# Kernel tuning notes

Hardware: AMD Instinct MI355X
Metric: run time of the kernel (lower is better)

## Reference

```python
import jax, jax.numpy as jnp
import numpy as np

B, S, D, NQ, NC, MC, K = 64, 200, 128, 50000, 1000, 4, 10
N = NQ + NC  # total graph nodes (concepts first, then questions, matching torch concat order)


def setup_inputs() -> dict:
    key = jax.random.key(0)
    ks = jax.random.split(key, 32)
    f = lambda i, shape: jax.random.normal(ks[i], shape, dtype=jnp.float32) * 0.02
    return {
        "emb_q": f(0, (NQ, D)), "emb_c": f(1, (NC, D)), "emb_r": f(2, (2, D)),
        "Wih1": f(3, (3 * D, 2 * D)), "Whh1": f(4, (3 * D, D)), "bih1": f(5, (3 * D,)), "bhh1": f(6, (3 * D,)),
        "Wih2": f(7, (3 * D, D)), "Whh2": f(8, (3 * D, D)), "bih2": f(9, (3 * D,)), "bhh2": f(10, (3 * D,)),
        "Wg1": f(11, (D, D)), "Wg2": f(12, (D, D)), "Wg3": f(13, (D, D)),
        "Wagg": f(14, (D, D)), "bagg": f(15, (D,)),
        "Wq": f(16, (D, D)), "bq": f(17, (D,)),
        "Wk": f(18, (D, D)), "bk": f(19, (D,)),
        "Ww": f(20, (1, 2 * D)), "bw": f(21, (1,)),
        "question_seq": jax.random.randint(ks[22], (B, S), 0, NQ),
        "correct_seq": jax.random.randint(ks[23], (B, S), 0, 2),
        "mask_seq": jnp.ones((B, S), dtype=jnp.int32),
        "q_table": jax.random.randint(ks[24], (NQ, MC), 0, NC),
    }


def _gru(x, h, Wih, Whh, bih, bhh):
    gi = x @ Wih.T + bih
    gh = h @ Whh.T + bhh
    i_r, i_z, i_n = jnp.split(gi, 3, axis=-1)
    h_r, h_z, h_n = jnp.split(gh, 3, axis=-1)
    r = jax.nn.sigmoid(i_r + h_r)
    z = jax.nn.sigmoid(i_z + h_z)
    n = jnp.tanh(i_n + r * h_n)
    return (1.0 - z) * n + z * h


def _sage_mean(x, src, dst, W):
    # SAGEConv4GIKT (eval): out = lin_r(mean_agg_over_neighbors + x), lin_r has no bias.
    agg = jax.ops.segment_sum(x[dst], src, num_segments=N)
    cnt = jax.ops.segment_sum(jnp.ones((src.shape[0], 1), x.dtype), src, num_segments=N)
    agg = agg / jnp.maximum(cnt, 1.0)
    return (agg + x) @ W.T


def reference(emb_q, emb_c, emb_r, Wih1, Whh1, bih1, bhh1, Wih2, Whh2, bih2, bhh2,
              Wg1, Wg2, Wg3, Wagg, bagg, Wq, bq, Wk, bk, Ww, bw,
              question_seq, correct_seq, mask_seq, q_table):
    # ---- GNN propagation over the full question-concept bipartite graph ----
    x = jnp.concatenate([emb_c, emb_q], axis=0)  # [N, D], concepts first
    q_glob = jnp.repeat(jnp.arange(NQ, dtype=q_table.dtype) + NC, MC)  # question global ids
    c_glob = q_table.reshape(-1)                                       # concept global ids
    x = _sage_mean(x, q_glob, c_glob, Wg1)  # q2c: aggregate at questions from concepts
    x = _sage_mean(x, c_glob, q_glob, Wg2)  # c2q: aggregate at concepts from questions
    x = _sage_mean(x, q_glob, c_glob, Wg3)  # q2c again
    x = jnp.tanh(x @ Wagg.T + bagg)

    tgrid = jnp.arange(S)

    def step(carry, inp):
        h1, h2, keyhist, statehist = carry
        t, q_t, r_t, m_t, q_next = inp
        m = (m_t != 0)[:, None]
        e_q = jnp.where(m, x[q_t + NC], emb_q[q_t])  # GNN emb where masked-in, raw emb otherwise
        e_r = emb_r[r_t]
        h1 = _gru(jnp.concatenate([e_q, e_r], axis=1), h1, Wih1, Whh1, bih1, bhh1)
        h2 = _gru(h1, h2, Wih2, Whh2, bih2, bhh2)
        statehist = statehist.at[:, t].set(h2)
        keyhist = keyhist.at[:, t].set(h2 @ Wk.T + bk)
        # queries: next question emb + its concept embs -> [B, MC+1, D]
        qc = jnp.concatenate([emb_q[q_next][:, None, :], emb_c[q_table[q_next]]], axis=1)
        aq = qc @ Wq.T + bq
        scores = jnp.einsum('bid,bjd->bij', aq, keyhist)  # [B, MC+1, S]
        scores = jnp.where((tgrid <= t)[None, None, :], scores, -1e9)
        flat = scores.reshape(B, -1)
        vals, idx = jax.lax.top_k(flat, K)  # top-k (query, state) pairs
        alpha = jax.nn.softmax(vals, axis=-1)
        i_idx = idx // S
        j_idx = idx % S
        q_sel = jnp.take_along_axis(qc, i_idx[:, :, None], axis=1)        # [B, K, D]
        s_sel = jnp.take_along_axis(statehist, j_idx[:, :, None], axis=1)  # [B, K, D]
        f = jax.nn.sigmoid(jnp.concatenate([q_sel, s_sel], axis=-1) @ Ww.T + bw)[..., 0]
        y = jnp.sum(alpha * f, axis=-1)  # [B]
        return (h1, h2, keyhist, statehist), y

    h0 = jnp.zeros((B, D), jnp.float32)
    carry = (h0, h0, jnp.zeros((B, S, D), jnp.float32), jnp.zeros((B, S, D), jnp.float32))
    xs = (jnp.arange(S - 1), question_seq[:, :-1].T, correct_seq[:, :-1].T,
          mask_seq[:, :-1].T, question_seq[:, 1:].T)
    _, ys = jax.lax.scan(step, carry, xs)
    y_hat = jnp.concatenate([jnp.zeros((B, 1), jnp.float32), ys.T], axis=1)  # predictions for t=1..S-1
    return y_hat
```

## Files before the change

### kernel.cpp

```cpp
#include <hip/hip_runtime.h>
#include <math.h>

#define Bz 64
#define Sz 200
#define Dz 128
#define NQz 50000
#define NCz 1000
#define MCz 4
#define Kz 10
#define Tz 199
#define NSz (Bz*Tz)
#define NEz (NQz*MCz)

__global__ void k_count(const int* __restrict__ qt, int* __restrict__ cnt) {
    int e = blockIdx.x*256 + threadIdx.x;
    if (e < NEz) atomicAdd(&cnt[qt[e]], 1);
}

__global__ void k_offs(const int* __restrict__ cnt, int* __restrict__ offs) {
    __shared__ int s[1024];
    int tid = threadIdx.x;
    s[tid] = (tid < NCz) ? cnt[tid] : 0;
    __syncthreads();
    for (int off = 1; off < 1024; off <<= 1) {
        int add = (tid >= off) ? s[tid - off] : 0;
        __syncthreads();
        s[tid] += add;
        __syncthreads();
    }
    if (tid < NCz) offs[tid + 1] = s[tid];
    if (tid == 0) offs[0] = 0;
}

__global__ void k_fill(const int* __restrict__ qt, const int* __restrict__ offs,
                       int* __restrict__ fill, int* __restrict__ edge_q) {
    int e = blockIdx.x*256 + threadIdx.x;
    if (e < NEz) {
        int c = qt[e];
        int pos = atomicAdd(&fill[c], 1);
        edge_q[offs[c] + pos] = e >> 2;
    }
}

__global__ void k_m2(const int* __restrict__ qt, const int* __restrict__ offs,
                     const int* __restrict__ edge_q,
                     const float* __restrict__ emb_q, const float* __restrict__ emb_c,
                     float* __restrict__ m2) {
    int c = blockIdx.x;
    int g = threadIdx.x >> 7;
    int d = threadIdx.x & 127;
    int e0 = offs[c], e1 = offs[c+1];
    float acc = 0.f;
    for (int e = e0 + g; e < e1; e += 4) {
        int q = edge_q[e];
        const int* t4 = qt + q*4;
        int c0 = t4[0], c1 = t4[1], c2 = t4[2], c3 = t4[3];
        acc += emb_q[q*128 + d]
             + 0.25f*(emb_c[c0*128+d] + emb_c[c1*128+d] + emb_c[c2*128+d] + emb_c[c3*128+d]);
    }
    __shared__ float ps[4][128];
    ps[g][d] = acc;
    __syncthreads();
    if (g == 0) {
        float tot = ps[0][d] + ps[1][d] + ps[2][d] + ps[3][d];
        float cn = (float)(e1 - e0);
        m2[c*128 + d] = tot / fmaxf(cn, 1.0f);
    }
}

template<bool TR>
__global__ void k_mm128(const float* __restrict__ X, const float* __restrict__ Y,
                        float* __restrict__ out) {
    int r = blockIdx.x, c = threadIdx.x;
    float acc = 0.f;
    for (int e = 0; e < 128; ++e) acc += X[r*128 + e] * Y[e*128 + c];
    if (TR) out[c*128 + r] = acc;
    else    out[r*128 + c] = acc;
}

__global__ void k_gr(const float* __restrict__ emb_r, const float* __restrict__ Wih1,
                     const float* __restrict__ bih1, float* __restrict__ gr) {
    int rt = threadIdx.x / 384, r = threadIdx.x % 384;
    float acc = bih1[r];
    for (int e = 0; e < 128; ++e) acc += emb_r[rt*128 + e] * Wih1[r*256 + 128 + e];
    gr[rt*384 + r] = acc;
}

__global__ void k_bkq(const float* __restrict__ Wq, const float* __restrict__ Wk,
                      const float* __restrict__ bq, const float* __restrict__ bk,
                      const float* __restrict__ Ww, const float* __restrict__ bw,
                      float* __restrict__ Bkq, float* __restrict__ biaskq) {
    int r = blockIdx.x, d = threadIdx.x;
    if (r < 128) {
        float acc = 0.f;
        for (int n = 0; n < 128; ++n) acc += Wq[n*128 + r] * Wk[n*128 + d];
        Bkq[r*128 + d] = acc;
        if (d == 0) {
            float b0 = 0.f;
            for (int n = 0; n < 128; ++n) b0 += Wq[n*128 + r] * bk[n];
            biaskq[r] = b0;
        }
    } else if (r == 128) {
        float acc = 0.f;
        for (int n = 0; n < 128; ++n) acc += bq[n] * Wk[n*128 + d];
        Bkq[128*128 + d] = acc;
        if (d == 0) {
            float c0 = 0.f;
            for (int n = 0; n < 128; ++n) c0 += bq[n] * bk[n];
            biaskq[128] = c0;
        }
    } else {
        Bkq[129*128 + d] = Ww[128 + d];
        if (d == 0) biaskq[129] = bw[0];
    }
}

__global__ void k_eq(const float* __restrict__ Mt_g, const float* __restrict__ bagg,
                     const float* __restrict__ emb_q, const float* __restrict__ emb_c,
                     const float* __restrict__ m2, const int* __restrict__ qseq,
                     const int* __restrict__ mseq, const int* __restrict__ qt,
                     float* __restrict__ eq) {
    __shared__ float Mt[128*128];
    __shared__ float ub[2][128];
    int tid = threadIdx.x;
    for (int i = tid; i < 128*128/4; i += 256)
        ((float4*)Mt)[i] = ((const float4*)Mt_g)[i];
    __syncthreads();
    int g = tid >> 7, d = tid & 127;
    for (int it = 0; it < 8; ++it) {
        int slot = blockIdx.x*16 + it*2 + g;
        int b = slot / Tz, t = slot % Tz;
        int q = qseq[b*Sz + t];
        int msk = mseq[b*Sz + t];
        if (msk) {
            const int* t4 = qt + q*4;
            int c0 = t4[0], c1 = t4[1], c2 = t4[2], c3 = t4[3];
            ub[g][d] = emb_q[q*128 + d]
                     + 0.5f *(emb_c[c0*128+d] + emb_c[c1*128+d] + emb_c[c2*128+d] + emb_c[c3*128+d])
                     + 0.25f*(m2[c0*128+d]  + m2[c1*128+d]  + m2[c2*128+d]  + m2[c3*128+d]);
        }
        __syncthreads();
        if (msk) {
            float acc = bagg[d];
            const float* urow = ub[g];
            for (int e = 0; e < 128; ++e) acc += Mt[e*128 + d] * urow[e];
            eq[slot*128 + d] = tanhf(acc);
        } else {
            eq[slot*128 + d] = emb_q[q*128 + d];
        }
        __syncthreads();
    }
}

__device__ __forceinline__ float bf_lo(unsigned u){ return __uint_as_float(u << 16); }
__device__ __forceinline__ float bf_hi(unsigned u){ return __uint_as_float(u & 0xffff0000u); }
__device__ __forceinline__ unsigned f2bf(float x){
    unsigned u = __float_as_uint(x);
    return (u + 0x7fffu + ((u >> 16) & 1u)) >> 16;
}
__device__ __forceinline__ unsigned pk2(float a, float b){
    return f2bf(a) | (f2bf(b) << 16);
}
__device__ __forceinline__ float rcpf(float x){ return __builtin_amdgcn_rcpf(x); }
__device__ __forceinline__ float sigm(float x){ return rcpf(1.f + __expf(-x)); }
__device__ __forceinline__ float tanh_fast(float x){
    float e = __expf(2.f*x);
    return 1.f - 2.f*rcpf(e + 1.f);
}

#if __has_builtin(__builtin_amdgcn_fdot2_f32_bf16)
typedef __attribute__((ext_vector_type(2))) short short2v;
__device__ __forceinline__ float bdot2(unsigned w, unsigned h, float acc) {
    return __builtin_amdgcn_fdot2_f32_bf16(__builtin_bit_cast(short2v, w),
                                           __builtin_bit_cast(short2v, h), acc, false);
}
#else
__device__ __forceinline__ float bdot2(unsigned w, unsigned h, float acc) {
    return acc + bf_lo(w)*bf_lo(h) + bf_hi(w)*bf_hi(h);
}
#endif

template<int MODE, int DOT2>
__global__ void k_gemm(const float* __restrict__ A, const float* __restrict__ Bm,
                       int ldb, int nB, float* __restrict__ C, int ldc,
                       const float* __restrict__ bias, const float* __restrict__ gr,
                       const int* __restrict__ cseq) {
    __shared__ int rtb[64];
    int tx = threadIdx.x, ty = threadIdx.y;
    int tid = ty*16 + tx;
    int m0 = blockIdx.x * 64;
    int n0 = blockIdx.y * 64;
    if (MODE == 1 && tid < 64) {
        int s = m0 + tid;
        int b = s / Tz, t = s % Tz;
        rtb[tid] = cseq[b*Sz + t];
    }
    float acc[4][4];
    #pragma unroll
    for (int i = 0; i < 4; ++i)
        #pragma unroll
        for (int j = 0; j < 4; ++j) acc[i][j] = 0.f;

    if (DOT2) {
        __shared__ unsigned As[64][17];
        __shared__ unsigned Bs[64][17];
        for (int kc = 0; kc < 128; kc += 32) {
            #pragma unroll
            for (int l = 0; l < 2; ++l) {
                int v = tid*2 + l;
                int row = v >> 3, c4 = (v & 7) << 2;
                int p0 = (kc + c4) >> 1 & 15;
                float4 av = *(const float4*)(A + (size_t)(m0+row)*128 + kc + c4);
                As[row][p0]   = pk2(av.x, av.y);
                As[row][p0+1] = pk2(av.z, av.w);
                int nrow = n0 + row;
                float4 bv = make_float4(0.f, 0.f, 0.f, 0.f);
                if (nrow < nB) bv = *(const float4*)(Bm + (size_t)nrow*ldb + kc + c4);
                Bs[row][p0]   = pk2(bv.x, bv.y);
                Bs[row][p0+1] = pk2(bv.z, bv.w);
            }
            __syncthreads();
            #pragma unroll 4
            for (int kp = 0; kp < 16; ++kp) {
                unsigned av[4], bv[4];
                #pragma unroll
                for (int i = 0; i < 4; ++i) av[i] = As[ty*4+i][kp];
                #pragma unroll
                for (int j = 0; j < 4; ++j) bv[j] = Bs[tx*4+j][kp];
                #pragma unroll
                for (int i = 0; i < 4; ++i)
                    #pragma unroll
                    for (int j = 0; j < 4; ++j) acc[i][j] = bdot2(av[i], bv[j], acc[i][j]);
            }
            __syncthreads();
        }
    } else {
        __shared__ float Asf[64][33];
        __shared__ float Bsf[64][33];
        for (int kc = 0; kc < 128; kc += 32) {
            #pragma unroll
            for (int l = 0; l < 2; ++l) {
                int v = tid*2 + l;
                int row = v >> 3, c4 = (v & 7) << 2;
                float4 av = *(const float4*)(A + (size_t)(m0+row)*128 + kc + c4);
                Asf[row][c4+0] = av.x; Asf[row][c4+1] = av.y; Asf[row][c4+2] = av.z; Asf[row][c4+3] = av.w;
                int nrow = n0 + row;
                float4 bv = make_float4(0.f, 0.f, 0.f, 0.f);
                if (nrow < nB) bv = *(const float4*)(Bm + (size_t)nrow*ldb + kc + c4);
                Bsf[row][c4+0] = bv.x; Bsf[row][c4+1] = bv.y; Bsf[row][c4+2] = bv.z; Bsf[row][c4+3] = bv.w;
            }
            __syncthreads();
            #pragma unroll 8
            for (int k = 0; k < 32; ++k) {
                float av[4], bv[4];
                #pragma unroll
                for (int i = 0; i < 4; ++i) av[i] = Asf[ty*4+i][k];
                #pragma unroll
                for (int j = 0; j < 4; ++j) bv[j] = Bsf[tx*4+j][k];
                #pragma unroll
                for (int i = 0; i < 4; ++i)
                    #pragma unroll
                    for (int j = 0; j < 4; ++j) acc[i][j] += av[i]*bv[j];
            }
            __syncthreads();
        }
    }
    #pragma unroll
    for (int i = 0; i < 4; ++i) {
        int s = m0 + ty*4 + i;
        #pragma unroll
        for (int j = 0; j < 4; ++j) {
            int col = n0 + tx*4 + j;
            if (col < nB) {
                float v = acc[i][j];
                if (MODE == 0) v += bias[col];
                else           v += gr[rtb[ty*4+i]*384 + col];
                C[(size_t)s*ldc + col] = v;
            }
        }
    }
}

__global__ void __launch_bounds__(384, 1)
k_scan(const float* __restrict__ gi, const float* __restrict__ Whh,
       const float* __restrict__ bhh, float* __restrict__ hout) {
    int b = blockIdx.x, tid = threadIdx.x;

    unsigned w[64];
    {
        const float4* w4 = (const float4*)(Whh + (size_t)tid*128);
        #pragma unroll
        for (int k = 0; k < 32; ++k) {
            float4 v = w4[k];
            w[2*k] = pk2(v.x, v.y); w[2*k+1] = pk2(v.z, v.w);
        }
    }
    float bb = bhh[tid];

    __shared__ unsigned hb[64];
    __shared__ float gh[384];
    if (tid < 64) hb[tid] = 0u;

    float g0=0.f,g1=0.f,g2=0.f,g3=0.f,g4=0.f,g5=0.f;
    if (tid < 64) {
        const float2* gp = (const float2*)(gi + (size_t)(b*Tz)*384);
        float2 x0 = gp[tid], x1 = gp[tid+64], x2 = gp[tid+128];
        g0=x0.x; g1=x0.y; g2=x1.x; g3=x1.y; g4=x2.x; g5=x2.y;
    }
    __syncthreads();

    const uint4* hv = (const uint4*)hb;

    for (int t = 0; t < Tz; ++t) {
        float n0=0.f,n1=0.f,n2=0.f,n3=0.f,n4=0.f,n5=0.f;
        if (tid < 64 && t + 1 < Tz) {
            const float2* gp = (const float2*)(gi + (size_t)(b*Tz + t + 1)*384);
            float2 x0 = gp[tid], x1 = gp[tid+64], x2 = gp[tid+128];
            n0=x0.x; n1=x0.y; n2=x1.x; n3=x1.y; n4=x2.x; n5=x2.y;
        }
        float a0=0.f, a1=0.f, a2=0.f, a3=0.f;
        #pragma unroll
        for (int k = 0; k < 8; ++k) {
            uint4 hp = hv[k];
            a0 = bdot2(w[4*k+0], hp.x, a0);
            a1 = bdot2(w[4*k+1], hp.y, a1);
            a2 = bdot2(w[4*k+2], hp.z, a2);
            a3 = bdot2(w[4*k+3], hp.w, a3);
        }
        gh[tid] = bb + ((a0+a1)+(a2+a3));
        __syncthreads();
        if (tid < 64) {
            int u = 2*tid;
            unsigned hp = hb[tid];
            float r0 = sigm(g0 + gh[u]);
            float r1 = sigm(g1 + gh[u+1]);
            float z0 = sigm(g2 + gh[u+128]);
            float z1 = sigm(g3 + gh[u+129]);
            float q0 = tanh_fast(g4 + r0*gh[u+256]);
            float q1 = tanh_fast(g5 + r1*gh[u+257]);
            float h0  = (1.f - z0)*q0 + z0*bf_lo(hp);
            float h1v = (1.f - z1)*q1 + z1*bf_hi(hp);
            hb[tid] = pk2(h0, h1v);
            ((float2*)(hout + (size_t)(b*Tz + t)*128))[tid] = make_float2(h0, h1v);
        }
        g0=n0; g1=n1; g2=n2; g3=n3; g4=n4; g5=n5;
        __syncthreads();
    }
}

__global__ void __launch_bounds__(256, 1)
k_attn(const float* __restrict__ kqb, const int* __restrict__ qseq,
       const int* __restrict__ qt, const float* __restrict__ emb_q,
       const float* __restrict__ emb_c, const float* __restrict__ Ww,
       float* __restrict__ out) {
    int wid  = threadIdx.x >> 6;
    int lane = threadIdx.x & 63;
    int b = blockIdx.y;
    int t = blockIdx.x*4 + wid;
    if (t > Tz - 1) t = Tz - 1;

    __shared__ float qc[4][5][128];
    __shared__ float gqs[4][5];
    int qn = qseq[b*Sz + t + 1];
    for (int idx = lane; idx < 5*128; idx += 64) {
        int i = idx / 128, d = idx & 127;
        const float* src = (i == 0) ? (emb_q + (size_t)qn*128)
                                    : (emb_c + (size_t)qt[qn*4 + (i-1)]*128);
        qc[wid][i][d] = src[d];
    }
    __syncthreads();
    {
        float w0 = Ww[lane], w1 = Ww[lane + 64];
        #pragma unroll
        for (int i = 0; i < 5; ++i) {
            float p = qc[wid][i][lane]*w0 + qc[wid][i][lane+64]*w1;
            #pragma unroll
            for (int off = 32; off >= 1; off >>= 1) p += __shfl_xor(p, off);
            if (lane == 0) gqs[wid][i] = p;
        }
    }
    __syncthreads();

    const float NEG = -3.402823466e38f;
    float sv[10]; int si[10];
    #pragma unroll
    for (int k = 0; k < 10; ++k) { sv[k] = NEG; si[k] = 0x7FFFFFFF; }

    for (int j = lane; j <= t; j += 64) {
        const float* krow = kqb + (size_t)(b*Tz + j)*132;
        const float4* kr4 = (const float4*)krow;
        float a0=0.f, a1=0.f, a2=0.f, a3=0.f, a4=0.f;
        #pragma unroll 4
        for (int c = 0; c < 32; ++c) {
            float4 kv = kr4[c];
            float4 q0 = ((const float4*)qc[wid][0])[c];
            float4 q1 = ((const float4*)qc[wid][1])[c];
            float4 q2 = ((const float4*)qc[wid][2])[c];
            float4 q3 = ((const float4*)qc[wid][3])[c];
            float4 q4 = ((const float4*)qc[wid][4])[c];
            a0 += q0.x*kv.x + q0.y*kv.y + q0.z*kv.z + q0.w*kv.w;
            a1 += q1.x*kv.x + q1.y*kv.y + q1.z*kv.z + q1.w*kv.w;
            a2 += q2.x*kv.x + q2.y*kv.y + q2.z*kv.z + q2.w*kv.w;
            a3 += q3.x*kv.x + q3.y*kv.y + q3.z*kv.z + q3.w*kv.w;
            a4 += q4.x*kv.x + q4.y*kv.y + q4.z*kv.z + q4.w*kv.w;
        }
        float kbj = krow[128];
        float scs[5] = {a0+kbj, a1+kbj, a2+kbj, a3+kbj, a4+kbj};
        #pragma unroll
        for (int i = 0; i < 5; ++i) {
            float cv = scs[i]; int ci = i*Sz + j;
            if (cv > sv[9] || (cv == sv[9] && ci < si[9])) {
                #pragma unroll
                for (int k = 0; k < 10; ++k) {
                    bool bet = (cv > sv[k]) || (cv == sv[k] && ci < si[k]);
                    float tvv = sv[k]; int tii = si[k];
                    if (bet) { sv[k] = cv; si[k] = ci; cv = tvv; ci = tii; }
                }
            }
        }
    }

    float vmax = 0.f, myv = 0.f; int myidx = 0x7FFFFFFF;
    #pragma unroll
    for (int rnd = 0; rnd < 10; ++rnd) {
        float v = sv[0]; int idx = si[0];
        #pragma unroll
        for (int off = 32; off >= 1; off >>= 1) {
            float ov = __shfl_xor(v, off);
            int   oi = __shfl_xor(idx, off);
            if (ov > v || (ov == v && oi < idx)) { v = ov; idx = oi; }
        }
        if (rnd == 0) vmax = v;
        if (lane == rnd) { myv = v; myidx = idx; }
        if (si[0] == idx) {
            #pragma unroll
            for (int k = 0; k < 9; ++k) { sv[k] = sv[k+1]; si[k] = si[k+1]; }
            sv[9] = NEG; si[9] = 0x7FFFFFFF;
        }
    }

    float num = 0.f, den = 0.f;
    if (lane < 10 && myidx != 0x7FFFFFFF) {
        float a = __expf(myv - vmax);
        int ik = myidx / Sz, jk = myidx % Sz;
        float gsj = kqb[(size_t)(b*Tz + jk)*132 + 129];
        float f = sigm(gqs[wid][ik] + gsj);
        num = a*f; den = a;
    }
    #pragma unroll
    for (int off = 32; off >= 1; off >>= 1) {
        num += __shfl_xor(num, off);
        den += __shfl_xor(den, off);
    }
    if (lane == 0) out[b*Sz + t + 1] = num/den;
}

static inline size_t alup(size_t x) { return (x + 255) & ~(size_t)255; }

extern "C" void kernel_launch(void* const* d_in, const int* in_sizes, int n_in,
                              void* d_out, int out_size, void* d_ws, size_t ws_size,
                              hipStream_t stream) {
    (void)in_sizes; (void)n_in; (void)ws_size;
    const float* emb_q = (const float*)d_in[0];
    const float* emb_c = (const float*)d_in[1];
    const float* emb_r = (const float*)d_in[2];
    const float* Wih1  = (const float*)d_in[3];
    const float* Whh1  = (const float*)d_in[4];
    const float* bih1  = (const float*)d_in[5];
    const float* bhh1  = (const float*)d_in[6];
    const float* Wih2  = (const float*)d_in[7];
    const float* Whh2  = (const float*)d_in[8];
    const float* bih2  = (const float*)d_in[9];
    const float* bhh2  = (const float*)d_in[10];
    const float* Wg1   = (const float*)d_in[11];
    const float* Wg2   = (const float*)d_in[12];
    const float* Wg3   = (const float*)d_in[13];
    const float* Wagg  = (const float*)d_in[14];
    const float* bagg  = (const float*)d_in[15];
    const float* Wq    = (const float*)d_in[16];
    const float* bq    = (const float*)d_in[17];
    const float* Wk    = (const float*)d_in[18];
    const float* bk    = (const float*)d_in[19];
    const float* Ww    = (const float*)d_in[20];
    const float* bw    = (const float*)d_in[21];
    const int* qseq    = (const int*)d_in[22];
    const int* cseq    = (const int*)d_in[23];
    const int* mseq    = (const int*)d_in[24];
    const int* qtab    = (const int*)d_in[25];
    float* out = (float*)d_out;

    char* p = (char*)d_ws;
    auto alloc = [&](size_t bytes) { char* r = p; p += alup(bytes); return r; };
    int*   cnt    = (int*)  alloc(4096);
    int*   fill   = (int*)  alloc(4096);
    int*   offs   = (int*)  alloc(1001*4);
    int*   edge_q = (int*)  alloc((size_t)NEz*4);
    float* m2     = (float*)alloc((size_t)NCz*128*4);
    float* T1     = (float*)alloc(128*128*4);
    float* T2     = (float*)alloc(128*128*4);
    float* Mt     = (float*)alloc(128*128*4);
    float* gr     = (float*)alloc(2*384*4);
    float* Bkq    = (float*)alloc(132*128*4);
    float* biaskq = (float*)alloc(132*4);
    float* eq     = (float*)alloc((size_t)NSz*128*4);
    float* gi1    = (float*)alloc((size_t)NSz*384*4);
    float* stateh = (float*)alloc((size_t)NSz*128*4);
    float* kqb    = (float*)alloc((size_t)NSz*132*4);
    float* h1all = eq;
    float* gi2   = gi1;

    hipMemsetAsync(cnt, 0, 8192, stream);
    hipMemsetAsync(d_out, 0, (size_t)out_size*4, stream);

    k_count<<<(NEz+255)/256, 256, 0, stream>>>(qtab, cnt);
    k_offs <<<1, 1024, 0, stream>>>(cnt, offs);
    k_fill <<<(NEz+255)/256, 256, 0, stream>>>(qtab, offs, fill, edge_q);
    k_m2   <<<NCz, 512, 0, stream>>>(qtab, offs, edge_q, emb_q, emb_c, m2);

    k_mm128<false><<<128, 128, 0, stream>>>(Wg2, Wg1, T1);
    k_mm128<false><<<128, 128, 0, stream>>>(Wg3, T1, T2);
    k_mm128<true> <<<128, 128, 0, stream>>>(Wagg, T2, Mt);
    k_gr  <<<1, 768, 0, stream>>>(emb_r, Wih1, bih1, gr);
    k_bkq <<<130, 128, 0, stream>>>(Wq, Wk, bq, bk, Ww, bw, Bkq, biaskq);

    k_eq  <<<NSz/16, 256, 0, stream>>>(Mt, bagg, emb_q, emb_c, m2, qseq, mseq, qtab, eq);

    k_gemm<1,1><<<dim3(NSz/64, 6), dim3(16,16), 0, stream>>>(eq, Wih1, 256, 384,
                                                             gi1, 384, nullptr, gr, cseq);
    k_scan<<<Bz, 384, 0, stream>>>(gi1, Whh1, bhh1, h1all);
    k_gemm<0,1><<<dim3(NSz/64, 6), dim3(16,16), 0, stream>>>(h1all, Wih2, 128, 384,
                                                             gi2, 384, bih2, nullptr, nullptr);
    k_scan<<<Bz, 384, 0, stream>>>(gi2, Whh2, bhh2, stateh);

    k_gemm<0,0><<<dim3(NSz/64, 3), dim3(16,16), 0, stream>>>(stateh, Bkq, 128, 132,
                                                             kqb, 132, biaskq, nullptr, nullptr);
    k_attn<<<dim3((Tz+3)/4, Bz), 256, 0, stream>>>(kqb, qseq, qtab, emb_q, emb_c, Ww, out);
}
```

Baseline: 675.4 us.

## Store key projections transposed per batch for coalesced attention score loads

The key/query projection GEMM now writes its output transposed, as [B][132][256 padded time], and no longer row-major per state. The attention kernel reads one dimension across lanes per load, so loads are coalesced and each lane accumulates up to four time slots in registers. Top-k insertion is done after the scores are computed. The risks are uncoalesced strided stores in the GEMM epilogue and higher register use from the 20 accumulators.

```diff
diff --git a/kernel.cpp b/kernel.cpp
--- a/kernel.cpp
+++ b/kernel.cpp
@@ -11,6 +11,7 @@
 #define Tz 199
 #define NSz (Bz*Tz)
 #define NEz (NQz*MCz)
+#define KTpad 256
 
 __global__ void k_count(const int* __restrict__ qt, int* __restrict__ cnt) {
     int e = blockIdx.x*256 + threadIdx.x;
@@ -268,14 +269,24 @@
     #pragma unroll
     for (int i = 0; i < 4; ++i) {
         int s = m0 + ty*4 + i;
-        #pragma unroll
-        for (int j = 0; j < 4; ++j) {
-            int col = n0 + tx*4 + j;
-            if (col < nB) {
-                float v = acc[i][j];
-                if (MODE == 0) v += bias[col];
-                else           v += gr[rtb[ty*4+i]*384 + col];
-                C[(size_t)s*ldc + col] = v;
+        if (MODE == 2) {
+            int bb = s / Tz, tt = s - ((int)(s / Tz))*Tz;
+            #pragma unroll
+            for (int j = 0; j < 4; ++j) {
+                int col = n0 + tx*4 + j;
+                if (col < nB)
+                    C[((size_t)bb*132 + col)*KTpad + tt] = acc[i][j] + bias[col];
+            }
+        } else {
+            #pragma unroll
+            for (int j = 0; j < 4; ++j) {
+                int col = n0 + tx*4 + j;
+                if (col < nB) {
+                    float v = acc[i][j];
+                    if (MODE == 0) v += bias[col];
+                    else           v += gr[rtb[ty*4+i]*384 + col];
+                    C[(size_t)s*ldc + col] = v;
+                }
             }
         }
     }
@@ -349,7 +360,7 @@
 }
 
 __global__ void __launch_bounds__(256, 1)
-k_attn(const float* __restrict__ kqb, const int* __restrict__ qseq,
+k_attn(const float* __restrict__ kqt, const int* __restrict__ qseq,
        const int* __restrict__ qt, const float* __restrict__ emb_q,
        const float* __restrict__ emb_c, const float* __restrict__ Ww,
        float* __restrict__ out) {
@@ -381,44 +392,79 @@
     }
     __syncthreads();
 
+    int nsl = (t >> 6) + 1;
+    const float* base = kqt + (size_t)b*(132*KTpad);
+
+    float a0[5], a1[5], a2[5], a3[5];
+    #pragma unroll
+    for (int i = 0; i < 5; ++i) { a0[i]=0.f; a1[i]=0.f; a2[i]=0.f; a3[i]=0.f; }
+
+    #pragma unroll 2
+    for (int c = 0; c < 32; ++c) {
+        float4 q0 = ((const float4*)qc[wid][0])[c];
+        float4 q1 = ((const float4*)qc[wid][1])[c];
+        float4 q2 = ((const float4*)qc[wid][2])[c];
+        float4 q3 = ((const float4*)qc[wid][3])[c];
+        float4 q4 = ((const float4*)qc[wid][4])[c];
+        #define ATTN_STEP(D, COMP)                                             \
+        {                                                                      \
+            const float* row = base + (size_t)(4*c + D)*KTpad;                 \
+            float k0 = row[lane];                                              \
+            a0[0] += q0.COMP*k0; a0[1] += q1.COMP*k0; a0[2] += q2.COMP*k0;     \
+            a0[3] += q3.COMP*k0; a0[4] += q4.COMP*k0;                          \
+            if (nsl > 1) {                                                     \
+                float k1 = row[lane+64];                                       \
+                a1[0] += q0.COMP*k1; a1[1] += q1.COMP*k1; a1[2] += q2.COMP*k1; \
+                a1[3] += q3.COMP*k1; a1[4] += q4.COMP*k1;                      \
+            }                                                                  \
+            if (nsl > 2) {                                                     \
+                float k2 = row[lane+128];                                      \
+                a2[0] += q0.COMP*k2; a2[1] += q1.COMP*k2; a2[2] += q2.COMP*k2; \
+                a2[3] += q3.COMP*k2; a2[4] += q4.COMP*k2;                      \
+            }                                                                  \
+            if (nsl > 3) {                                                     \
+                float k3 = row[lane+192];                                      \
+                a3[0] += q0.COMP*k3; a3[1] += q1.COMP*k3; a3[2] += q2.COMP*k3; \
+                a3[3] += q3.COMP*k3; a3[4] += q4.COMP*k3;                      \
+            }                                                                  \
+        }
+        ATTN_STEP(0, x) ATTN_STEP(1, y) ATTN_STEP(2, z) ATTN_STEP(3, w)
+        #undef ATTN_STEP
+    }
+
     const float NEG = -3.402823466e38f;
     float sv[10]; int si[10];
     #pragma unroll
     for (int k = 0; k < 10; ++k) { sv[k] = NEG; si[k] = 0x7FFFFFFF; }
 
-    for (int j = lane; j <= t; j += 64) {
-        const float* krow = kqb + (size_t)(b*Tz + j)*132;
-        const float4* kr4 = (const float4*)krow;
-        float a0=0.f, a1=0.f, a2=0.f, a3=0.f, a4=0.f;
-        #pragma unroll 4
-        for (int c = 0; c < 32; ++c) {
-            float4 kv = kr4[c];
-            float4 q0 = ((const float4*)qc[wid][0])[c];
-            float4 q1 = ((const float4*)qc[wid][1])[c];
-            float4 q2 = ((const float4*)qc[wid][2])[c];
-            float4 q3 = ((const float4*)qc[wid][3])[c];
-            float4 q4 = ((const float4*)qc[wid][4])[c];
-            a0 += q0.x*kv.x + q0.y*kv.y + q0.z*kv.z + q0.w*kv.w;
-            a1 += q1.x*kv.x + q1.y*kv.y + q1.z*kv.z + q1.w*kv.w;
-            a2 += q2.x*kv.x + q2.y*kv.y + q2.z*kv.z + q2.w*kv.w;
-            a3 += q3.x*kv.x + q3.y*kv.y + q3.z*kv.z + q3.w*kv.w;
-            a4 += q4.x*kv.x + q4.y*kv.y + q4.z*kv.z + q4.w*kv.w;
-        }
-        float kbj = krow[128];
-        float scs[5] = {a0+kbj, a1+kbj, a2+kbj, a3+kbj, a4+kbj};
-        #pragma unroll
-        for (int i = 0; i < 5; ++i) {
-            float cv = scs[i]; int ci = i*Sz + j;
-            if (cv > sv[9] || (cv == sv[9] && ci < si[9])) {
-                #pragma unroll
-                for (int k = 0; k < 10; ++k) {
-                    bool bet = (cv > sv[k]) || (cv == sv[k] && ci < si[k]);
-                    float tvv = sv[k]; int tii = si[k];
-                    if (bet) { sv[k] = cv; si[k] = ci; cv = tvv; ci = tii; }
-                }
-            }
-        }
-    }
+    auto ins = [&](float cv, int ci) {
+        if (cv > sv[9] || (cv == sv[9] && ci < si[9])) {
+            #pragma unroll
+            for (int k = 0; k < 10; ++k) {
+                bool bet = (cv > sv[k]) || (cv == sv[k] && ci < si[k]);
+                float tv = sv[k]; int ti = si[k];
+                if (bet) { sv[k] = cv; si[k] = ci; cv = tv; ci = ti; }
+            }
+        }
+    };
+    const float* kbr = base + 128*KTpad;
+    {
+        int j = lane;
+        if (j <= t) {
+            float kb = kbr[j];
+            #pragma unroll
+            for (int i = 0; i < 5; ++i) ins(a0[i] + kb, i*Sz + j);
+        }
+    }
+    if (nsl > 1) { int j = lane+64;  if (j <= t) { float kb = kbr[j];
+        #pragma unroll
+        for (int i = 0; i < 5; ++i) ins(a1[i] + kb, i*Sz + j); } }
+    if (nsl > 2) { int j = lane+128; if (j <= t) { float kb = kbr[j];
+        #pragma unroll
+        for (int i = 0; i < 5; ++i) ins(a2[i] + kb, i*Sz + j); } }
+    if (nsl > 3) { int j = lane+192; if (j <= t) { float kb = kbr[j];
+        #pragma unroll
+        for (int i = 0; i < 5; ++i) ins(a3[i] + kb, i*Sz + j); } }
 
     float vmax = 0.f, myv = 0.f; int myidx = 0x7FFFFFFF;
     #pragma unroll
@@ -443,7 +489,7 @@
     if (lane < 10 && myidx != 0x7FFFFFFF) {
         float a = __expf(myv - vmax);
         int ik = myidx / Sz, jk = myidx % Sz;
-        float gsj = kqb[(size_t)(b*Tz + jk)*132 + 129];
+        float gsj = base[129*KTpad + jk];
         float f = sigm(gqs[wid][ik] + gsj);
         num = a*f; den = a;
     }
@@ -505,7 +551,7 @@
     float* eq     = (float*)alloc((size_t)NSz*128*4);
     float* gi1    = (float*)alloc((size_t)NSz*384*4);
     float* stateh = (float*)alloc((size_t)NSz*128*4);
-    float* kqb    = (float*)alloc((size_t)NSz*132*4);
+    float* kqt    = (float*)alloc((size_t)Bz*132*KTpad*4);
     float* h1all = eq;
     float* gi2   = gi1;
 
@@ -532,7 +578,7 @@
                                                              gi2, 384, bih2, nullptr, nullptr);
     k_scan<<<Bz, 384, 0, stream>>>(gi2, Whh2, bhh2, stateh);
 
-    k_gemm<0,0><<<dim3(NSz/64, 3), dim3(16,16), 0, stream>>>(stateh, Bkq, 128, 132,
-                                                             kqb, 132, biaskq, nullptr, nullptr);
-    k_attn<<<dim3((Tz+3)/4, Bz), 256, 0, stream>>>(kqb, qseq, qtab, emb_q, emb_c, Ww, out);
-}
+    k_gemm<2,0><<<dim3(NSz/64, 3), dim3(16,16), 0, stream>>>(stateh, Bkq, 128, 132,
+                                                             kqt, 0, biaskq, nullptr, nullptr);
+    k_attn<<<dim3((Tz+3)/4, Bz), 256, 0, stream>>>(kqt, qseq, qtab, emb_q, emb_c, Ww, out);
+}
```

After: 723.6 us. +7.1%, slower.
